# Optimization experiments

Hardware: AMD Instinct MI355X
Metric: run time of the kernel (lower is better)

The kernel has to match this reference:

```python
import jax, jax.numpy as jnp
import numpy as np

N_NODES = 10000
N_EDGES = 640000
HID = 128


def setup_inputs() -> dict:
    key = jax.random.key(0)
    ks = jax.random.split(key, 8)
    h = jax.random.normal(ks[0], (N_NODES, HID), dtype=jnp.float32)
    edge_index = jax.random.randint(ks[1], (2, N_EDGES), 0, N_NODES, dtype=jnp.int64)
    edge_attr = jax.random.normal(ks[2], (N_EDGES, 1), dtype=jnp.float32)
    s1 = 1.0 / np.sqrt(2 * HID + 1)
    s2 = 1.0 / np.sqrt(HID)
    s3 = 1.0 / np.sqrt(2 * HID)
    return {
        "h": h,
        "edge_index": edge_index,
        "edge_attr": edge_attr,
        "msg_w1": jax.random.normal(ks[3], (2 * HID + 1, HID), dtype=jnp.float32) * s1,
        "msg_b1": jnp.zeros((HID,), dtype=jnp.float32),
        "msg_w2": jax.random.normal(ks[4], (HID, HID), dtype=jnp.float32) * s2,
        "msg_b2": jnp.zeros((HID,), dtype=jnp.float32),
        "upd_w1": jax.random.normal(ks[5], (2 * HID, HID), dtype=jnp.float32) * s3,
        "upd_b1": jnp.zeros((HID,), dtype=jnp.float32),
        "upd_w2": jax.random.normal(ks[6], (HID, HID), dtype=jnp.float32) * s2,
        "upd_b2": jnp.zeros((HID,), dtype=jnp.float32),
    }


def reference(h, edge_index, edge_attr, msg_w1, msg_b1, msg_w2, msg_b2,
              upd_w1, upd_b1, upd_w2, upd_b2):
    src, dst = edge_index[0], edge_index[1]
    # gather -> concat: [E, 2*HID+1]
    m_in = jnp.concatenate([h[src], h[dst], edge_attr], axis=1)
    # message MLP
    msg = jax.nn.relu(m_in @ msg_w1 + msg_b1) @ msg_w2 + msg_b2
    # scatter-add over destination nodes: [N, HID]
    agg = jax.ops.segment_sum(msg, dst, num_segments=h.shape[0])
    # update MLP with residual
    upd_in = jnp.concatenate([h, agg], axis=1)
    upd = jax.nn.relu(upd_in @ upd_w1 + upd_b1) @ upd_w2 + upd_b2
    return h + upd
```

## Files before the change

kernel.cpp:

```cpp
#include <hip/hip_runtime.h>
#include <hip/hip_bf16.h>

#define HID 128
#define NNODES 10000
#define NEDGES 640000
#define NBIN 625
#define NPB 16
#define BINCAP 1408

typedef __attribute__((ext_vector_type(8))) short bf16x8;
typedef __attribute__((ext_vector_type(4))) float f32x4;

__device__ inline short f2bf(float f) {
  unsigned u = __builtin_bit_cast(unsigned, f);
  u = (u + 0x7fffu + ((u >> 16) & 1u)) >> 16;
  return (short)u;
}
__device__ inline float bf2f(unsigned short u) {
  unsigned ui = ((unsigned)u) << 16;
  return __builtin_bit_cast(float, ui);
}

__global__ void k_zero(int* __restrict__ g) {
  int i = blockIdx.x * 256 + threadIdx.x;
  if (i < NBIN) g[i] = 0;
}

__global__ __launch_bounds__(256) void k_partA(
    const int* __restrict__ eidxraw, const float* __restrict__ ea,
    int* __restrict__ gbinctr, uint2* __restrict__ part,
    const float* __restrict__ h,
    const float* __restrict__ mw1, const float* __restrict__ mw2,
    const float* __restrict__ uw1, const float* __restrict__ uw2,
    short* __restrict__ pW2, short* __restrict__ pU1, short* __restrict__ pU2,
    const float* __restrict__ b1,
    short* __restrict__ Xs, short* __restrict__ cvecbf) {
  const int bid = blockIdx.x;
  const int tid = threadIdx.x;
  if (bid < 313) {
    __shared__ int cur[NBIN];
    for (int t = tid; t < NBIN; t += 256) cur[t] = 0;
    __syncthreads();
    bool is64 = true;
#pragma unroll
    for (int k = 0; k < 16; ++k) is64 = is64 && (eidxraw[2 * k + 1] == 0);
    int sv[8], dv[8];
    float av[8];
    bool ok[8];
#pragma unroll
    for (int k = 0; k < 8; ++k) {
      int e = bid * 2048 + k * 256 + tid;
      ok[k] = (e < NEDGES);
      int ec = ok[k] ? e : 0;
      sv[k] = is64 ? eidxraw[2 * ec] : eidxraw[ec];
      dv[k] = is64 ? eidxraw[2 * (NEDGES + ec)] : eidxraw[NEDGES + ec];
      av[k] = ea[ec];
      if (ok[k]) atomicAdd(&cur[dv[k] >> 4], 1);
    }
    __syncthreads();
    for (int t = tid; t < NBIN; t += 256) {
      int hcnt = cur[t];
      int g = 0;
      if (hcnt) g = atomicAdd(&gbinctr[t], hcnt);
      cur[t] = t * BINCAP + g;
    }
    __syncthreads();
#pragma unroll
    for (int k = 0; k < 8; ++k) {
      if (ok[k]) {
        int b = dv[k] >> 4;
        int pos = atomicAdd(&cur[b], 1);
        if (pos < (b + 1) * BINCAP)
          part[pos] = make_uint2(((unsigned)dv[k] << 16) | (unsigned)sv[k],
                                 __builtin_bit_cast(unsigned, av[k]));
      }
    }
  } else if (bid < 345) {
    int pb = bid - 313;
    const float* W; short* out; int t;
    if (pb < 8)       { W = mw2; out = pW2; t = pb * 256; }
    else if (pb < 24) { W = uw1; out = pU1; t = (pb - 8) * 256; }
    else              { W = uw2; out = pU2; t = (pb - 24) * 256; }
    t += tid;
    int l = t & 63, nt = (t >> 6) & 7, kt = t >> 9;
    int col = nt * 16 + (l & 15);
    int k0 = kt * 32 + ((l >> 4) << 3);
    bf16x8 o;
#pragma unroll
    for (int j = 0; j < 8; ++j) o[j] = f2bf(W[(k0 + j) * HID + col]);
    reinterpret_cast<bf16x8*>(out)[t] = o;
  } else {
    const int wv = tid >> 6, l = tid & 63;
    const int lr = l & 15, lg = l >> 4;
    const int rbase = (bid - 345) * 64 + wv * 16;
    int rA = rbase + lr;
    if (rA > NNODES - 1) rA = NNODES - 1;
    const float* hrow = h + (size_t)rA * HID;
    const float* W1a = mw1;
    const float* W1b = mw1 + 128 * HID;

    const f32x4 zero = {0.f, 0.f, 0.f, 0.f};
    f32x4 accA[8], accB[8];
#pragma unroll
    for (int nt = 0; nt < 8; ++nt) { accA[nt] = zero; accB[nt] = zero; }
#pragma unroll
    for (int kt = 0; kt < 4; ++kt) {
      f32x4 a0 = *reinterpret_cast<const f32x4*>(hrow + kt * 32 + lg * 8);
      f32x4 a1 = *reinterpret_cast<const f32x4*>(hrow + kt * 32 + lg * 8 + 4);
      bf16x8 af;
#pragma unroll
      for (int j = 0; j < 4; ++j) { af[j] = f2bf(a0[j]); af[4 + j] = f2bf(a1[j]); }
      const int k0 = kt * 32 + lg * 8;
#pragma unroll
      for (int nt = 0; nt < 8; ++nt) {
        const int col = nt * 16 + lr;
        bf16x8 bfa, bfb;
#pragma unroll
        for (int j = 0; j < 8; ++j) {
          bfa[j] = f2bf(W1a[(k0 + j) * HID + col]);
          bfb[j] = f2bf(W1b[(k0 + j) * HID + col]);
        }
        accA[nt] = __builtin_amdgcn_mfma_f32_16x16x32_bf16(af, bfa, accA[nt], 0, 0, 0);
        accB[nt] = __builtin_amdgcn_mfma_f32_16x16x32_bf16(af, bfb, accB[nt], 0, 0, 0);
      }
    }
#pragma unroll
    for (int nt = 0; nt < 8; ++nt) {
      const int col = nt * 16 + lr;
      const float bb = b1[col];
#pragma unroll
      for (int i = 0; i < 4; ++i) {
        int row = rbase + lg * 4 + i;
        if (row < NNODES) {
          ((unsigned short*)Xs)[row * HID + col] = (unsigned short)f2bf(accA[nt][i]);
          ((unsigned short*)cvecbf)[row * HID + col] = (unsigned short)f2bf(accB[nt][i] + bb);
        }
      }
    }
  }
}

__global__ __launch_bounds__(256) void k_merged(
    const short* __restrict__ Xs, const uint2* __restrict__ part,
    const int* __restrict__ gbinctr, const short* __restrict__ cvecbf,
    const float* __restrict__ w1raw, const float* __restrict__ hf,
    const short* __restrict__ pW2, const float* __restrict__ b2,
    const short* __restrict__ pU1, const float* __restrict__ bu1,
    const short* __restrict__ pU2, const float* __restrict__ bu2,
    float* __restrict__ out) {
  __shared__ __align__(16) uint2 eLDS[BINCAP];
  __shared__ __align__(16) short ldsR[NPB][136];
  __shared__ int cntL[NPB], offsL[NPB], curL[NPB];
  short* ldsA = (short*)eLDS;
  short* ldsB = ((short*)eLDS) + NPB * 136;
  const int b = blockIdx.x;
  const int tid = threadIdx.x;
  const int wv = tid >> 6, l = tid & 63;
  const int lr = l & 15, lg = l >> 4;
  const int nb = b * NPB;

  if (tid < NPB) cntL[tid] = 0;
  __syncthreads();
  int count = gbinctr[b];
  if (count > BINCAP) count = BINCAP;
  const uint2* seg = part + b * BINCAP;
  uint2 st[6];
  int sl[6];
#pragma unroll
  for (int r = 0; r < 6; ++r) {
    int i = tid + r * 256;
    if (i < count) {
      st[r] = seg[i];
      sl[r] = (int)(st[r].x >> 16) - nb;
      atomicAdd(&cntL[sl[r]], 1);
    }
  }
  __syncthreads();
  if (tid < NPB) {
    int v = cntL[tid];
    int x = v;
#pragma unroll
    for (int d = 1; d < NPB; d <<= 1) {
      int y = __shfl_up(x, d);
      if (tid >= d) x += y;
    }
    offsL[tid] = x - v;
    curL[tid] = x - v;
  }
  __syncthreads();
#pragma unroll
  for (int r = 0; r < 6; ++r) {
    int i = tid + r * 256;
    if (i < count) {
      int pos = atomicAdd(&curL[sl[r]], 1);
      eLDS[pos] = make_uint2(st[r].x & 0xFFFFu, st[r].y);
    }
  }
  __syncthreads();

  float wl[8];
  {
    f32x4 w0 = *reinterpret_cast<const f32x4*>(w1raw + 256 * HID + lr * 8);
    f32x4 w1v = *reinterpret_cast<const f32x4*>(w1raw + 256 * HID + lr * 8 + 4);
#pragma unroll
    for (int k = 0; k < 4; ++k) { wl[k] = w0[k]; wl[k + 4] = w1v[k]; }
  }

#pragma unroll
  for (int q = 0; q < 4; ++q) {
    const int local = wv * 4 + q;
    const int node = nb + local;
    const int off = offsL[local];
    const int deg = cntL[local];
    float cv[8];
    {
      bf16x8 cvv = *reinterpret_cast<const bf16x8*>(cvecbf + node * HID + lr * 8);
#pragma unroll
      for (int k = 0; k < 8; ++k) cv[k] = bf2f((unsigned short)cvv[k]);
    }
    float acc[8];
#pragma unroll
    for (int k = 0; k < 8; ++k) acc[k] = 0.f;

    for (int j0 = 0; j0 < deg; j0 += 16) {
      bf16x8 xs_[4];
      float av_[4];
      bool val_[4];
#pragma unroll
      for (int u = 0; u < 4; ++u) {
        int j = j0 + u * 4 + lg;
        val_[u] = (j < deg);
        int jc = val_[u] ? j : deg - 1;
        uint2 ent = eLDS[off + jc];
        av_[u] = __builtin_bit_cast(float, ent.y);
        xs_[u] = *reinterpret_cast<const bf16x8*>(Xs + (int)ent.x * HID + lr * 8);
      }
#pragma unroll
      for (int u = 0; u < 4; ++u) {
#pragma unroll
        for (int k = 0; k < 8; ++k) {
          float v = fmaxf(fmaf(av_[u], wl[k], bf2f((unsigned short)xs_[u][k]) + cv[k]), 0.f);
          acc[k] += val_[u] ? v : 0.f;
        }
      }
    }
#pragma unroll
    for (int k = 0; k < 8; ++k) {
      acc[k] += __shfl_xor(acc[k], 16);
      acc[k] += __shfl_xor(acc[k], 32);
    }
    if (l < 16) {
      bf16x8 r;
#pragma unroll
      for (int k = 0; k < 8; ++k) r[k] = f2bf(acc[k]);
      *reinterpret_cast<bf16x8*>(&ldsR[local][lr * 8]) = r;
    }
  }
  __syncthreads();

  const int nt0 = wv * 2;
  const f32x4 zero = {0.f, 0.f, 0.f, 0.f};

  f32x4 acc0[2] = {zero, zero};
#pragma unroll
  for (int kt = 0; kt < 4; ++kt) {
    bf16x8 af = *reinterpret_cast<const bf16x8*>(&ldsR[lr][kt * 32 + lg * 8]);
#pragma unroll
    for (int t = 0; t < 2; ++t) {
      bf16x8 bf = reinterpret_cast<const bf16x8*>(pW2)[(kt * 8 + nt0 + t) * 64 + l];
      acc0[t] = __builtin_amdgcn_mfma_f32_16x16x32_bf16(af, bf, acc0[t], 0, 0, 0);
    }
  }
#pragma unroll
  for (int t = 0; t < 2; ++t) {
    const int col = (nt0 + t) * 16 + lr;
    const float bb = b2[col];
#pragma unroll
    for (int i = 0; i < 4; ++i) {
      int row = lg * 4 + i;
      float degr = (float)cntL[row];
      ldsA[row * 136 + col] = f2bf(acc0[t][i] + degr * bb);
    }
  }
  __syncthreads();

  f32x4 acc1[2] = {zero, zero};
  const float* hrow = hf + (size_t)(nb + lr) * HID;
#pragma unroll
  for (int kt = 0; kt < 8; ++kt) {
    bf16x8 af;
    if (kt < 4) {
      f32x4 a0 = *reinterpret_cast<const f32x4*>(hrow + kt * 32 + lg * 8);
      f32x4 a1 = *reinterpret_cast<const f32x4*>(hrow + kt * 32 + lg * 8 + 4);
#pragma unroll
      for (int j = 0; j < 4; ++j) { af[j] = f2bf(a0[j]); af[4 + j] = f2bf(a1[j]); }
    } else {
      af = *reinterpret_cast<const bf16x8*>(&ldsA[lr * 136 + (kt - 4) * 32 + lg * 8]);
    }
#pragma unroll
    for (int t = 0; t < 2; ++t) {
      bf16x8 bf = reinterpret_cast<const bf16x8*>(pU1)[(kt * 8 + nt0 + t) * 64 + l];
      acc1[t] = __builtin_amdgcn_mfma_f32_16x16x32_bf16(af, bf, acc1[t], 0, 0, 0);
    }
  }
#pragma unroll
  for (int t = 0; t < 2; ++t) {
    const int col = (nt0 + t) * 16 + lr;
    const float bb = bu1[col];
#pragma unroll
    for (int i = 0; i < 4; ++i)
      ldsB[(lg * 4 + i) * 136 + col] = f2bf(fmaxf(acc1[t][i] + bb, 0.f));
  }
  __syncthreads();

  f32x4 acc2[2] = {zero, zero};
#pragma unroll
  for (int kt = 0; kt < 4; ++kt) {
    bf16x8 af = *reinterpret_cast<const bf16x8*>(&ldsB[lr * 136 + kt * 32 + lg * 8]);
#pragma unroll
    for (int t = 0; t < 2; ++t) {
      bf16x8 bf = reinterpret_cast<const bf16x8*>(pU2)[(kt * 8 + nt0 + t) * 64 + l];
      acc2[t] = __builtin_amdgcn_mfma_f32_16x16x32_bf16(af, bf, acc2[t], 0, 0, 0);
    }
  }
#pragma unroll
  for (int t = 0; t < 2; ++t) {
    const int col = (nt0 + t) * 16 + lr;
    const float bb = bu2[col];
#pragma unroll
    for (int i = 0; i < 4; ++i) {
      int row = nb + lg * 4 + i;
      out[row * HID + col] = hf[row * HID + col] + acc2[t][i] + bb;
    }
  }
}

extern "C" void kernel_launch(void* const* d_in, const int* in_sizes, int n_in,
                              void* d_out, int out_size, void* d_ws, size_t ws_size,
                              hipStream_t stream) {
  const float* h    = (const float*)d_in[0];
  const int*   eidx = (const int*)d_in[1];
  const float* ea   = (const float*)d_in[2];
  const float* mw1  = (const float*)d_in[3];
  const float* mb1  = (const float*)d_in[4];
  const float* mw2  = (const float*)d_in[5];
  const float* mb2  = (const float*)d_in[6];
  const float* uw1  = (const float*)d_in[7];
  const float* ub1  = (const float*)d_in[8];
  const float* uw2  = (const float*)d_in[9];
  const float* ub2  = (const float*)d_in[10];
  float* out = (float*)d_out;

  char* ws = (char*)d_ws;
  uint2* part    = (uint2*)(ws + 0);
  short* Xs      = (short*)(ws + 7040000);
  short* cvecbf  = (short*)(ws + 9600000);
  int*   gbinctr = (int*)(ws + 12160000);
  short* pW2     = (short*)(ws + 12162560);
  short* pU1     = (short*)(ws + 12195328);
  short* pU2     = (short*)(ws + 12260864);

  k_zero<<<3, 256, 0, stream>>>(gbinctr);
  k_partA<<<502, 256, 0, stream>>>(eidx, ea, gbinctr, part, h, mw1, mw2, uw1, uw2,
                                   pW2, pU1, pU2, mb1, Xs, cvecbf);
  k_merged<<<NBIN, 256, 0, stream>>>(Xs, part, gbinctr, cvecbf, mw1, h,
                                     pW2, mb2, pU1, ub1, pU2, ub2, out);
}
```

Measured before the change: 64.67 us.

## Replace global-atomic bin partition with per-block sorted slabs and offset tables

The edge partition no longer uses global atomic bin counters or a zeroing kernel. Each of 250 scatter blocks now counting-sorts its 2560 edges by destination bin in LDS, writes the sorted slab coalesced, and records per-bin offsets. The consumer kernel prefix-scans those 250 offsets and gathers its bin's edges from every slab, then re-sorts by node locally. This removes a launch and global atomics but adds many small scattered reads per consumer block plus serial block-wide scans. The edge loop also gains an unpredicated fast path for full groups of 16 edges.

```diff
diff --git a/kernel.cpp b/kernel.cpp
--- a/kernel.cpp
+++ b/kernel.cpp
@@ -7,6 +7,10 @@
 #define NBIN 625
 #define NPB 16
 #define BINCAP 1408
+#define SCATB 250
+#define EPT 10
+#define SLAB 2560
+#define PBOS 640
 
 typedef __attribute__((ext_vector_type(8))) short bf16x8;
 typedef __attribute__((ext_vector_type(4))) float f32x4;
@@ -21,78 +25,93 @@
   return __builtin_bit_cast(float, ui);
 }
 
-__global__ void k_zero(int* __restrict__ g) {
-  int i = blockIdx.x * 256 + threadIdx.x;
-  if (i < NBIN) g[i] = 0;
-}
-
 __global__ __launch_bounds__(256) void k_partA(
     const int* __restrict__ eidxraw, const float* __restrict__ ea,
-    int* __restrict__ gbinctr, uint2* __restrict__ part,
+    uint2* __restrict__ part, int* __restrict__ pbo,
     const float* __restrict__ h,
     const float* __restrict__ mw1, const float* __restrict__ mw2,
     const float* __restrict__ uw1, const float* __restrict__ uw2,
     short* __restrict__ pW2, short* __restrict__ pU1, short* __restrict__ pU2,
     const float* __restrict__ b1,
     short* __restrict__ Xs, short* __restrict__ cvecbf) {
+  __shared__ int histL[NBIN + 1];
+  __shared__ int offsL[NBIN + 1];
+  __shared__ int spL[256];
+  __shared__ __align__(16) uint2 slab[SLAB];
   const int bid = blockIdx.x;
   const int tid = threadIdx.x;
-  if (bid < 313) {
-    __shared__ int cur[NBIN];
-    for (int t = tid; t < NBIN; t += 256) cur[t] = 0;
+
+  if (bid < SCATB) {
+    for (int i = tid; i < NBIN + 1; i += 256) histL[i] = 0;
     __syncthreads();
     bool is64 = true;
 #pragma unroll
     for (int k = 0; k < 16; ++k) is64 = is64 && (eidxraw[2 * k + 1] == 0);
-    int sv[8], dv[8];
-    float av[8];
-    bool ok[8];
-#pragma unroll
-    for (int k = 0; k < 8; ++k) {
-      int e = bid * 2048 + k * 256 + tid;
-      ok[k] = (e < NEDGES);
-      int ec = ok[k] ? e : 0;
-      sv[k] = is64 ? eidxraw[2 * ec] : eidxraw[ec];
-      dv[k] = is64 ? eidxraw[2 * (NEDGES + ec)] : eidxraw[NEDGES + ec];
-      av[k] = ea[ec];
-      if (ok[k]) atomicAdd(&cur[dv[k] >> 4], 1);
-    }
-    __syncthreads();
-    for (int t = tid; t < NBIN; t += 256) {
-      int hcnt = cur[t];
-      int g = 0;
-      if (hcnt) g = atomicAdd(&gbinctr[t], hcnt);
-      cur[t] = t * BINCAP + g;
-    }
-    __syncthreads();
-#pragma unroll
-    for (int k = 0; k < 8; ++k) {
-      if (ok[k]) {
-        int b = dv[k] >> 4;
-        int pos = atomicAdd(&cur[b], 1);
-        if (pos < (b + 1) * BINCAP)
-          part[pos] = make_uint2(((unsigned)dv[k] << 16) | (unsigned)sv[k],
-                                 __builtin_bit_cast(unsigned, av[k]));
-      }
-    }
-  } else if (bid < 345) {
-    int pb = bid - 313;
-    const float* W; short* out; int t;
-    if (pb < 8)       { W = mw2; out = pW2; t = pb * 256; }
-    else if (pb < 24) { W = uw1; out = pU1; t = (pb - 8) * 256; }
-    else              { W = uw2; out = pU2; t = (pb - 24) * 256; }
+    unsigned pk[EPT];
+    float av[EPT];
+    const int ebase = bid * SLAB;
+#pragma unroll
+    for (int r = 0; r < EPT; ++r) {
+      int e = ebase + r * 256 + tid;
+      int sv = is64 ? eidxraw[2 * e] : eidxraw[e];
+      int dv = is64 ? eidxraw[2 * (NEDGES + e)] : eidxraw[NEDGES + e];
+      pk[r] = ((unsigned)dv << 16) | (unsigned)sv;
+      av[r] = ea[e];
+      atomicAdd(&histL[dv >> 4], 1);
+    }
+    __syncthreads();
+    int c0 = 0, c1 = 0, c2 = 0;
+    {
+      int b0 = tid * 3;
+      if (b0 < NBIN) c0 = histL[b0];
+      if (b0 + 1 < NBIN) c1 = histL[b0 + 1];
+      if (b0 + 2 < NBIN) c2 = histL[b0 + 2];
+    }
+    int s = c0 + c1 + c2;
+    spL[tid] = s;
+    __syncthreads();
+    for (int d = 1; d < 256; d <<= 1) {
+      int v = (tid >= d) ? spL[tid - d] : 0;
+      __syncthreads();
+      spL[tid] += v;
+      __syncthreads();
+    }
+    int run = spL[tid] - s;
+    {
+      int b0 = tid * 3;
+      if (b0 < NBIN)     { offsL[b0] = run;     histL[b0] = run;     run += c0; }
+      if (b0 + 1 < NBIN) { offsL[b0 + 1] = run; histL[b0 + 1] = run; run += c1; }
+      if (b0 + 2 < NBIN) { offsL[b0 + 2] = run; histL[b0 + 2] = run; }
+    }
+    if (tid == 255) offsL[NBIN] = spL[255];
+    __syncthreads();
+#pragma unroll
+    for (int r = 0; r < EPT; ++r) {
+      int bin = pk[r] >> 20;
+      int pos = atomicAdd(&histL[bin], 1);
+      slab[pos] = make_uint2(pk[r], __builtin_bit_cast(unsigned, av[r]));
+    }
+    __syncthreads();
+    for (int i = tid; i < SLAB; i += 256) part[bid * SLAB + i] = slab[i];
+    for (int i = tid; i < NBIN + 1; i += 256) pbo[bid * PBOS + i] = offsL[i];
+  } else if (bid < 282) {
+    int pb = bid - SCATB;
+    const float* W; short* outp; int t;
+    if (pb < 8)       { W = mw2; outp = pW2; t = pb * 256; }
+    else if (pb < 24) { W = uw1; outp = pU1; t = (pb - 8) * 256; }
+    else              { W = uw2; outp = pU2; t = (pb - 24) * 256; }
     t += tid;
-    int l = t & 63, nt = (t >> 6) & 7, kt = t >> 9;
-    int col = nt * 16 + (l & 15);
-    int k0 = kt * 32 + ((l >> 4) << 3);
+    int ll = t & 63, nt = (t >> 6) & 7, kt = t >> 9;
+    int col = nt * 16 + (ll & 15);
+    int k0 = kt * 32 + ((ll >> 4) << 3);
     bf16x8 o;
 #pragma unroll
     for (int j = 0; j < 8; ++j) o[j] = f2bf(W[(k0 + j) * HID + col]);
-    reinterpret_cast<bf16x8*>(out)[t] = o;
+    reinterpret_cast<bf16x8*>(outp)[t] = o;
   } else {
     const int wv = tid >> 6, l = tid & 63;
     const int lr = l & 15, lg = l >> 4;
-    const int rbase = (bid - 345) * 64 + wv * 16;
+    const int rbase = (bid - 282) * 64 + wv * 16;
     int rA = rbase + lr;
     if (rA > NNODES - 1) rA = NNODES - 1;
     const float* hrow = h + (size_t)rA * HID;
@@ -142,59 +161,68 @@
 
 __global__ __launch_bounds__(256) void k_merged(
     const short* __restrict__ Xs, const uint2* __restrict__ part,
-    const int* __restrict__ gbinctr, const short* __restrict__ cvecbf,
+    const int* __restrict__ pbo, const short* __restrict__ cvecbf,
     const float* __restrict__ w1raw, const float* __restrict__ hf,
     const short* __restrict__ pW2, const float* __restrict__ b2,
     const short* __restrict__ pU1, const float* __restrict__ bu1,
     const short* __restrict__ pU2, const float* __restrict__ bu2,
     float* __restrict__ out) {
-  __shared__ __align__(16) uint2 eLDS[BINCAP];
+  __shared__ __align__(16) uint2 eraw[BINCAP];
+  __shared__ __align__(16) uint2 efin[BINCAP];
   __shared__ __align__(16) short ldsR[NPB][136];
-  __shared__ int cntL[NPB], offsL[NPB], curL[NPB];
-  short* ldsA = (short*)eLDS;
-  short* ldsB = ((short*)eLDS) + NPB * 136;
+  __shared__ int spL[256];
+  __shared__ int cnt16[NPB], off16[NPB], cur16[NPB];
+  short* ldsA = (short*)eraw;
+  short* ldsB = (short*)efin;
   const int b = blockIdx.x;
   const int tid = threadIdx.x;
   const int wv = tid >> 6, l = tid & 63;
   const int lr = l & 15, lg = l >> 4;
   const int nb = b * NPB;
 
-  if (tid < NPB) cntL[tid] = 0;
-  __syncthreads();
-  int count = gbinctr[b];
-  if (count > BINCAP) count = BINCAP;
-  const uint2* seg = part + b * BINCAP;
-  uint2 st[6];
-  int sl[6];
-#pragma unroll
-  for (int r = 0; r < 6; ++r) {
-    int i = tid + r * 256;
-    if (i < count) {
-      st[r] = seg[i];
-      sl[r] = (int)(st[r].x >> 16) - nb;
-      atomicAdd(&cntL[sl[r]], 1);
-    }
-  }
-  __syncthreads();
+  if (tid < NPB) cnt16[tid] = 0;
+  int o0 = 0, cnt_t = 0;
+  if (tid < SCATB) {
+    o0 = pbo[tid * PBOS + b];
+    cnt_t = pbo[tid * PBOS + b + 1] - o0;
+  }
+  spL[tid] = cnt_t;
+  __syncthreads();
+  for (int d = 1; d < 256; d <<= 1) {
+    int v = (tid >= d) ? spL[tid - d] : 0;
+    __syncthreads();
+    spL[tid] += v;
+    __syncthreads();
+  }
+  const int base = spL[tid] - cnt_t;
+  for (int i = 0; i < cnt_t; ++i) {
+    uint2 ent = part[tid * SLAB + o0 + i];
+    int pos = base + i;
+    if (pos < BINCAP) {
+      atomicAdd(&cnt16[(int)(ent.x >> 16) & 15], 1);
+      eraw[pos] = ent;
+    }
+  }
+  __syncthreads();
+  int total = spL[255];
+  if (total > BINCAP) total = BINCAP;
   if (tid < NPB) {
-    int v = cntL[tid];
+    int v = cnt16[tid];
     int x = v;
 #pragma unroll
     for (int d = 1; d < NPB; d <<= 1) {
       int y = __shfl_up(x, d);
       if (tid >= d) x += y;
     }
-    offsL[tid] = x - v;
-    curL[tid] = x - v;
-  }
-  __syncthreads();
-#pragma unroll
-  for (int r = 0; r < 6; ++r) {
-    int i = tid + r * 256;
-    if (i < count) {
-      int pos = atomicAdd(&curL[sl[r]], 1);
-      eLDS[pos] = make_uint2(st[r].x & 0xFFFFu, st[r].y);
-    }
+    off16[tid] = x - v;
+    cur16[tid] = x - v;
+  }
+  __syncthreads();
+  for (int i = tid; i < total; i += 256) {
+    uint2 ent = eraw[i];
+    int local = (int)(ent.x >> 16) & 15;
+    int pos = atomicAdd(&cur16[local], 1);
+    efin[pos] = make_uint2(ent.x & 0xFFFFu, ent.y);
   }
   __syncthreads();
 
@@ -210,8 +238,8 @@
   for (int q = 0; q < 4; ++q) {
     const int local = wv * 4 + q;
     const int node = nb + local;
-    const int off = offsL[local];
-    const int deg = cntL[local];
+    const int off = off16[local];
+    const int deg = cnt16[local];
     float cv[8];
     {
       bf16x8 cvv = *reinterpret_cast<const bf16x8*>(cvecbf + node * HID + lr * 8);
@@ -222,27 +250,42 @@
 #pragma unroll
     for (int k = 0; k < 8; ++k) acc[k] = 0.f;
 
-    for (int j0 = 0; j0 < deg; j0 += 16) {
+    const int deg16 = deg & ~15;
+    for (int j0 = 0; j0 < deg16; j0 += 16) {
+      bf16x8 xs_[4];
+      float av_[4];
+#pragma unroll
+      for (int u = 0; u < 4; ++u) {
+        uint2 ent = efin[off + j0 + u * 4 + lg];
+        av_[u] = __builtin_bit_cast(float, ent.y);
+        xs_[u] = *reinterpret_cast<const bf16x8*>(Xs + (int)ent.x * HID + lr * 8);
+      }
+#pragma unroll
+      for (int u = 0; u < 4; ++u)
+#pragma unroll
+        for (int k = 0; k < 8; ++k)
+          acc[k] += fmaxf(fmaf(av_[u], wl[k], bf2f((unsigned short)xs_[u][k]) + cv[k]), 0.f);
+    }
+    if (deg16 < deg) {
       bf16x8 xs_[4];
       float av_[4];
       bool val_[4];
 #pragma unroll
       for (int u = 0; u < 4; ++u) {
-        int j = j0 + u * 4 + lg;
+        int j = deg16 + u * 4 + lg;
         val_[u] = (j < deg);
-        int jc = val_[u] ? j : deg - 1;
-        uint2 ent = eLDS[off + jc];
+        int jc = val_[u] ? j : (deg > 0 ? deg - 1 : 0);
+        uint2 ent = efin[off + jc];
         av_[u] = __builtin_bit_cast(float, ent.y);
         xs_[u] = *reinterpret_cast<const bf16x8*>(Xs + (int)ent.x * HID + lr * 8);
       }
 #pragma unroll
-      for (int u = 0; u < 4; ++u) {
+      for (int u = 0; u < 4; ++u)
 #pragma unroll
         for (int k = 0; k < 8; ++k) {
           float v = fmaxf(fmaf(av_[u], wl[k], bf2f((unsigned short)xs_[u][k]) + cv[k]), 0.f);
           acc[k] += val_[u] ? v : 0.f;
         }
-      }
     }
 #pragma unroll
     for (int k = 0; k < 8; ++k) {
@@ -278,7 +321,7 @@
 #pragma unroll
     for (int i = 0; i < 4; ++i) {
       int row = lg * 4 + i;
-      float degr = (float)cntL[row];
+      float degr = (float)cnt16[row];
       ldsA[row * 136 + col] = f2bf(acc0[t][i] + degr * bb);
     }
   }
@@ -352,17 +395,16 @@
   float* out = (float*)d_out;
 
   char* ws = (char*)d_ws;
-  uint2* part    = (uint2*)(ws + 0);
-  short* Xs      = (short*)(ws + 7040000);
-  short* cvecbf  = (short*)(ws + 9600000);
-  int*   gbinctr = (int*)(ws + 12160000);
-  short* pW2     = (short*)(ws + 12162560);
-  short* pU1     = (short*)(ws + 12195328);
-  short* pU2     = (short*)(ws + 12260864);
-
-  k_zero<<<3, 256, 0, stream>>>(gbinctr);
-  k_partA<<<502, 256, 0, stream>>>(eidx, ea, gbinctr, part, h, mw1, mw2, uw1, uw2,
+  uint2* part   = (uint2*)(ws + 0);
+  int*   pbo    = (int*)(ws + 5120000);
+  short* Xs     = (short*)(ws + 5760000);
+  short* cvecbf = (short*)(ws + 8320000);
+  short* pW2    = (short*)(ws + 10880000);
+  short* pU1    = (short*)(ws + 10912768);
+  short* pU2    = (short*)(ws + 10978304);
+
+  k_partA<<<439, 256, 0, stream>>>(eidx, ea, part, pbo, h, mw1, mw2, uw1, uw2,
                                    pW2, pU1, pU2, mb1, Xs, cvecbf);
-  k_merged<<<NBIN, 256, 0, stream>>>(Xs, part, gbinctr, cvecbf, mw1, h,
+  k_merged<<<NBIN, 256, 0, stream>>>(Xs, part, pbo, cvecbf, mw1, h,
                                      pW2, mb2, pU1, ub1, pU2, ub2, out);
 }
```

New measurement: 61.71 us. 1.05x faster.
